# Optimization experiments

Measured on AMD Instinct MI355X. Metric: run time of the kernel, lower is better.

The kernel has to match this reference:

```python
import jax, jax.numpy as jnp
import numpy as np
from jax import lax

WIN = 9  # box-filter window per spatial dim
PAD = WIN // 2


def _box_sum(x, filt):
    # x: [N,1,D,H,W]; uniform ones filter -> local sums, 'same' padding
    return lax.conv_general_dilated(
        x, filt, window_strides=(1, 1, 1),
        padding=[(PAD, PAD)] * 3,
        dimension_numbers=("NCDHW", "OIDHW", "NCDHW"))


def l_ncc(I, J):
    filt = jnp.ones((1, 1, WIN, WIN, WIN), dtype=I.dtype)
    win_size = float(WIN ** 3)
    I_sum = _box_sum(I, filt)
    J_sum = _box_sum(J, filt)
    I2_sum = _box_sum(I * I, filt)
    J2_sum = _box_sum(J * J, filt)
    IJ_sum = _box_sum(I * J, filt)
    u_I = I_sum / win_size
    u_J = J_sum / win_size
    cross = IJ_sum - u_J * I_sum - u_I * J_sum + u_I * u_J * win_size
    I_var = I2_sum - 2.0 * u_I * I_sum + u_I * u_I * win_size
    J_var = J2_sum - 2.0 * u_J * J_sum + u_J * u_J * win_size
    cc = cross * cross / (I_var * J_var + 1e-5)
    return 1.0 - jnp.mean(cc)


def l_mse(y_true, y_pred):
    return jnp.mean((y_true - y_pred) ** 2)


def l_smooth(s):
    # squared forward differences along the three spatial axes of [N,C,D,H,W]
    dy = s[..., 1:, :, :] - s[..., :-1, :, :]
    dx = s[..., :, 1:, :] - s[..., :, :-1, :]
    dz = s[..., :, :, 1:] - s[..., :, :, :-1]
    d = jnp.mean(dx * dx) + jnp.mean(dy * dy) + jnp.mean(dz * dz)
    return d / 3.0


def setup_inputs() -> dict:
    key = jax.random.key(0)
    k1, k2, k3, k4 = jax.random.split(key, 4)
    shp = (2, 1, 128, 128, 128)
    return {
        "imgsA": jax.random.uniform(k1, shp, dtype=jnp.float32),
        "recon_A": jax.random.uniform(k2, shp, dtype=jnp.float32),
        "warped_BA": jax.random.uniform(k3, shp, dtype=jnp.float32),
        "flow_BA": jax.random.normal(k4, (2, 3, 128, 128, 128), dtype=jnp.float32),
    }


def reference(imgsA, recon_A, warped_BA, flow_BA):
    ncc_loss = l_ncc(warped_BA, imgsA)
    mse_loss = l_mse(imgsA, recon_A)
    smooth_loss = l_smooth(flow_BA)
    return (ncc_loss, mse_loss, smooth_loss)
```

## Files before the change

### kernel.cpp

```cpp
#include <hip/hip_runtime.h>

#define VOL   4194304
#define FLOWN 12582912
#define SMCNT 12484608.0f
#define WIN_INV (1.0f / 729.0f)

__device__ __forceinline__ void block_reduce_atomic(float v, float* red, float* dst) {
#pragma unroll
    for (int off = 32; off; off >>= 1) v += __shfl_down(v, off);
    if ((threadIdx.x & 63) == 0) red[threadIdx.x >> 6] = v;
    __syncthreads();
    if (threadIdx.x == 0) atomicAdd(dst, red[0] + red[1] + red[2] + red[3]);
}

struct __align__(16) NccLds {
    float wst[2][5][16][28];
    float hst[2][5][16][16];
};

#define WSLIDE(c, X0,X1,X2,X3,X4,X5,X6,X7,X8,X9,X10,X11)                   \
    {                                                                      \
        const float o0 = X0+X1+X2+X3+X4+X5+X6+X7+X8;                       \
        const float o1 = o0 - X0 + X9;                                     \
        const float o2 = o1 - X1 + X10;                                    \
        const float o3 = o2 - X2 + X11;                                    \
        L->wst[wpl][c][wq4 + 0][wrr] = o0;                                 \
        L->wst[wpl][c][wq4 + 1][wrr] = o1;                                 \
        L->wst[wpl][c][wq4 + 2][wrr] = o2;                                 \
        L->wst[wpl][c][wq4 + 3][wrr] = o3;                                 \
    }

__device__ void ncc_block(const float* __restrict__ I, const float* __restrict__ J,
                          float* __restrict__ acc, NccLds* L, float* red, int nb) {
    const int wt = nb & 7, ht = (nb >> 3) & 7, dc = (nb >> 6) & 7, n = nb >> 9;
    const int w0 = wt << 4, h0 = ht << 4, d0 = dc << 4;
    const int tid = threadIdx.x;
    const int th = tid & 15;
    const int tw = tid >> 4;

    const int wpl = tid / 96;
    const int wit = tid - wpl * 96;
    const int wrr = wit >> 2;
    const int wq4 = (wit & 3) << 2;
    const int gh  = h0 - 4 + wrr;
    const int gwb = w0 + wq4 - 4;

    float hist[5][9];
#pragma unroll
    for (int c = 0; c < 5; ++c)
#pragma unroll
        for (int k = 0; k < 9; ++k) hist[c][k] = 0.f;
    float S[5] = {0.f, 0.f, 0.f, 0.f, 0.f};
    float local = 0.f;
    const long nbase = (long)n * 2097152;

    for (int pp = 0; pp < 12; ++pp) {
        {
            const int s  = 2 * pp + wpl;
            const int dp = d0 - 4 + s;
            if (tid < 192 && (unsigned)dp < 128u) {
                const float4 z4 = make_float4(0.f, 0.f, 0.f, 0.f);
                float4 i0 = z4, i1 = z4, i2 = z4, j0 = z4, j1 = z4, j2 = z4;
                if ((unsigned)gh < 128u) {
                    const float* Ip = I + nbase + (long)dp * 16384 + gh * 128 + gwb;
                    const float* Jp = J + nbase + (long)dp * 16384 + gh * 128 + gwb;
                    if (gwb >= 0)   { i0 = *(const float4*)Ip;       j0 = *(const float4*)Jp; }
                    i1 = *(const float4*)(Ip + 4);                   j1 = *(const float4*)(Jp + 4);
                    if (gwb <= 116) { i2 = *(const float4*)(Ip + 8); j2 = *(const float4*)(Jp + 8); }
                }
                WSLIDE(0, i0.x,i0.y,i0.z,i0.w, i1.x,i1.y,i1.z,i1.w, i2.x,i2.y,i2.z,i2.w)
                WSLIDE(1, j0.x,j0.y,j0.z,j0.w, j1.x,j1.y,j1.z,j1.w, j2.x,j2.y,j2.z,j2.w)
                WSLIDE(2, i0.x*i0.x,i0.y*i0.y,i0.z*i0.z,i0.w*i0.w,
                          i1.x*i1.x,i1.y*i1.y,i1.z*i1.z,i1.w*i1.w,
                          i2.x*i2.x,i2.y*i2.y,i2.z*i2.z,i2.w*i2.w)
                WSLIDE(3, j0.x*j0.x,j0.y*j0.y,j0.z*j0.z,j0.w*j0.w,
                          j1.x*j1.x,j1.y*j1.y,j1.z*j1.z,j1.w*j1.w,
                          j2.x*j2.x,j2.y*j2.y,j2.z*j2.z,j2.w*j2.w)
                WSLIDE(4, i0.x*j0.x,i0.y*j0.y,i0.z*j0.z,i0.w*j0.w,
                          i1.x*j1.x,i1.y*j1.y,i1.z*j1.z,i1.w*j1.w,
                          i2.x*j2.x,i2.y*j2.y,i2.z*j2.z,i2.w*j2.w)
            }
        }
        __syncthreads();
#pragma unroll
        for (int rep = 0; rep < 3; ++rep) {
            int id = -1;
            if (rep < 2) id = tid + rep * 256;
            else if (tid >= 128) id = 384 + tid;
            if (id >= 0 && id < 640) {
                const int pl = id >= 320;
                const int r2 = id - pl * 320;
                const int c  = r2 >> 6;
                const int w  = (r2 >> 2) & 15;
                const int qh = r2 & 3;
                const int dp = d0 - 4 + 2 * pp + pl;
                if ((unsigned)dp < 128u) {
                    const float* sp = &L->wst[pl][c][w][qh << 2];
                    const float4 a0 = *(const float4*)sp;
                    const float4 a1 = *(const float4*)(sp + 4);
                    const float4 a2 = *(const float4*)(sp + 8);
                    const float o0 = a0.x+a0.y+a0.z+a0.w+a1.x+a1.y+a1.z+a1.w+a2.x;
                    const float o1 = o0 - a0.x + a2.y;
                    const float o2 = o1 - a0.y + a2.z;
                    const float o3 = o2 - a0.z + a2.w;
                    *(float4*)&L->hst[pl][c][w][qh << 2] = make_float4(o0, o1, o2, o3);
                }
            }
        }
        __syncthreads();
        {
            const int dp0 = d0 - 4 + 2 * pp;
            float p0[5], p1[5];
            if ((unsigned)dp0 < 128u) {
#pragma unroll
                for (int c = 0; c < 5; ++c) p0[c] = L->hst[0][c][tw][th];
            } else {
#pragma unroll
                for (int c = 0; c < 5; ++c) p0[c] = 0.f;
            }
            if ((unsigned)(dp0 + 1) < 128u) {
#pragma unroll
                for (int c = 0; c < 5; ++c) p1[c] = L->hst[1][c][tw][th];
            } else {
#pragma unroll
                for (int c = 0; c < 5; ++c) p1[c] = 0.f;
            }
#pragma unroll
            for (int c = 0; c < 5; ++c) S[c] += p0[c] - hist[c][8];
            if (pp >= 4) {
                const float cross = S[4] - S[0] * S[1] * WIN_INV;
                const float iv    = S[2] - S[0] * S[0] * WIN_INV;
                const float jv    = S[3] - S[1] * S[1] * WIN_INV;
                local += cross * cross / (iv * jv + 1e-5f);
            }
#pragma unroll
            for (int c = 0; c < 5; ++c) S[c] += p1[c] - hist[c][7];
            if (pp >= 4) {
                const float cross = S[4] - S[0] * S[1] * WIN_INV;
                const float iv    = S[2] - S[0] * S[0] * WIN_INV;
                const float jv    = S[3] - S[1] * S[1] * WIN_INV;
                local += cross * cross / (iv * jv + 1e-5f);
            }
#pragma unroll
            for (int c = 0; c < 5; ++c) {
#pragma unroll
                for (int k = 8; k >= 2; --k) hist[c][k] = hist[c][k - 2];
                hist[c][1] = p0[c];
                hist[c][0] = p1[c];
            }
        }
    }
    block_reduce_atomic(local, red, &acc[0]);
}

__device__ void mse_block(const float4* __restrict__ a, const float4* __restrict__ b,
                          float* __restrict__ acc, float* red, int mb) {
    float local = 0.f;
    for (int i = mb * 256 + threadIdx.x; i < VOL / 4; i += 512 * 256) {
        const float4 x = a[i], y = b[i];
        const float d0 = x.x - y.x, d1 = x.y - y.y, d2 = x.z - y.z, d3 = x.w - y.w;
        local += d0 * d0 + d1 * d1 + d2 * d2 + d3 * d3;
    }
    block_reduce_atomic(local, red, &acc[1]);
}

__device__ void smooth_block(const float4* __restrict__ s,
                             float* __restrict__ acc, float* red, int sb) {
    float local = 0.f;
    for (int f = sb * 256 + threadIdx.x; f < FLOWN / 4; f += 2048 * 256) {
        const int w4 = f & 31, h = (f >> 5) & 127, d = (f >> 12) & 127;
        const float4 v = s[f];
        const float t1 = v.y - v.x, t2 = v.z - v.y, t3 = v.w - v.z;
        local += t1 * t1 + t2 * t2 + t3 * t3;
        if (w4 < 31) {
            const float nx = ((const float*)s)[4 * f + 4];
            const float t = nx - v.w;
            local += t * t;
        }
        if (h < 127) {
            const float4 nh = s[f + 32];
            const float u0 = nh.x - v.x, u1 = nh.y - v.y, u2 = nh.z - v.z, u3 = nh.w - v.w;
            local += u0 * u0 + u1 * u1 + u2 * u2 + u3 * u3;
        }
        if (d < 127) {
            const float4 nd = s[f + 4096];
            const float u0 = nd.x - v.x, u1 = nd.y - v.y, u2 = nd.z - v.z, u3 = nd.w - v.w;
            local += u0 * u0 + u1 * u1 + u2 * u2 + u3 * u3;
        }
    }
    block_reduce_atomic(local, red, &acc[2]);
}

__global__ __launch_bounds__(256) void fused_k(const float* __restrict__ imgsA,
                                               const float* __restrict__ recon,
                                               const float* __restrict__ warped,
                                               const float* __restrict__ flow,
                                               float* __restrict__ acc) {
    __shared__ NccLds Lsh;
    __shared__ float red[4];
    const int g = blockIdx.x;
    if (g < 1024) {
        ncc_block(warped, imgsA, acc, &Lsh, red, g);
    } else {
        const int x = g - 1024;
        const int q = x / 5, r = x - q * 5;
        if (r == 0) mse_block((const float4*)imgsA, (const float4*)recon, acc, red, q);
        else        smooth_block((const float4*)flow, acc, red, q * 4 + (r - 1));
    }
}

__global__ void fin_k(const float* __restrict__ acc, float* __restrict__ out) {
    if (threadIdx.x == 0) {
        out[0] = 1.0f - acc[0] * (1.0f / (float)VOL);
        out[1] = acc[1] * (1.0f / (float)VOL);
        out[2] = acc[2] * (1.0f / (3.0f * SMCNT));
    }
}

extern "C" void kernel_launch(void* const* d_in, const int* in_sizes, int n_in,
                              void* d_out, int out_size, void* d_ws, size_t ws_size,
                              hipStream_t stream) {
    const float* imgsA  = (const float*)d_in[0];
    const float* recon  = (const float*)d_in[1];
    const float* warped = (const float*)d_in[2];
    const float* flow   = (const float*)d_in[3];
    float* out = (float*)d_out;
    float* acc = (float*)d_ws;

    hipMemsetAsync(d_ws, 0, 16, stream);
    fused_k<<<3584, 256, 0, stream>>>(imgsA, recon, warped, flow, acc);
    fin_k<<<1, 64, 0, stream>>>(acc, out);
}
```

Measured before the change: 82.00 us.

## Process four depth planes per iteration with wave-local H pass and prefetch

The NCC box filter now gives each of the four waves its own depth plane, so four planes are handled per iteration instead of two. Each wave does the W-slide and the H-slide on its own plane using only a wave-local LDS wait, which removes one block-wide barrier per step. Global loads for the next plane group are issued into registers before the barrier, so memory traffic overlaps with the depth accumulation. Blocks are also interleaved so NCC blocks alternate with MSE and smooth blocks, and launch bounds request three blocks per CU. The cost is higher register use from the prefetch buffers and a larger LDS footprint, which could limit occupancy.

```diff
diff --git a/kernel.cpp b/kernel.cpp
--- a/kernel.cpp
+++ b/kernel.cpp
@@ -14,8 +14,8 @@
 }
 
 struct __align__(16) NccLds {
-    float wst[2][5][16][28];
-    float hst[2][5][16][16];
+    float wst[4][5][16][24];
+    float hst[4][5][16][16];
 };
 
 #define WSLIDE(c, X0,X1,X2,X3,X4,X5,X6,X7,X8,X9,X10,X11)                   \
@@ -24,10 +24,17 @@
         const float o1 = o0 - X0 + X9;                                     \
         const float o2 = o1 - X1 + X10;                                    \
         const float o3 = o2 - X2 + X11;                                    \
-        L->wst[wpl][c][wq4 + 0][wrr] = o0;                                 \
-        L->wst[wpl][c][wq4 + 1][wrr] = o1;                                 \
-        L->wst[wpl][c][wq4 + 2][wrr] = o2;                                 \
-        L->wst[wpl][c][wq4 + 3][wrr] = o3;                                 \
+        L->wst[wv][c][wq4 + 0][wrr] = o0;                                  \
+        L->wst[wv][c][wq4 + 1][wrr] = o1;                                  \
+        L->wst[wv][c][wq4 + 2][wrr] = o2;                                  \
+        L->wst[wv][c][wq4 + 3][wrr] = o3;                                  \
+    }
+
+#define EMIT {                                                             \
+        const float cross = S[4] - S[0] * S[1] * WIN_INV;                  \
+        const float iv    = S[2] - S[0] * S[0] * WIN_INV;                  \
+        const float jv    = S[3] - S[1] * S[1] * WIN_INV;                  \
+        local += cross * cross / (iv * jv + 1e-5f);                       \
     }
 
 __device__ void ncc_block(const float* __restrict__ I, const float* __restrict__ J,
@@ -35,15 +42,10 @@
     const int wt = nb & 7, ht = (nb >> 3) & 7, dc = (nb >> 6) & 7, n = nb >> 9;
     const int w0 = wt << 4, h0 = ht << 4, d0 = dc << 4;
     const int tid = threadIdx.x;
-    const int th = tid & 15;
-    const int tw = tid >> 4;
-
-    const int wpl = tid / 96;
-    const int wit = tid - wpl * 96;
-    const int wrr = wit >> 2;
-    const int wq4 = (wit & 3) << 2;
-    const int gh  = h0 - 4 + wrr;
-    const int gwb = w0 + wq4 - 4;
+    const int wv   = tid >> 6;
+    const int lane = tid & 63;
+    const int th = tid & 15, tw = (tid >> 4) & 15;
+    const int hw = (lane >> 2) & 15, hq = lane & 3;
 
     float hist[5][9];
 #pragma unroll
@@ -54,101 +56,103 @@
     float local = 0.f;
     const long nbase = (long)n * 2097152;
 
-    for (int pp = 0; pp < 12; ++pp) {
-        {
-            const int s  = 2 * pp + wpl;
-            const int dp = d0 - 4 + s;
-            if (tid < 192 && (unsigned)dp < 128u) {
-                const float4 z4 = make_float4(0.f, 0.f, 0.f, 0.f);
-                float4 i0 = z4, i1 = z4, i2 = z4, j0 = z4, j1 = z4, j2 = z4;
+    float4 Ri0[2], Ri1[2], Ri2[2], Rj0[2], Rj1[2], Rj2[2];
+
+    auto load_plane = [&](int s4) {
+        const int dp = d0 - 4 + s4 + wv;
+        const bool v = (unsigned)dp < 128u;
+#pragma unroll
+        for (int r = 0; r < 2; ++r) {
+            const float4 z4 = make_float4(0.f, 0.f, 0.f, 0.f);
+            Ri0[r] = Ri1[r] = Ri2[r] = Rj0[r] = Rj1[r] = Rj2[r] = z4;
+            const int item = lane + (r << 6);
+            if (v && item < 96) {
+                const int rr = item >> 2, q4 = (item & 3) << 2;
+                const int gh = h0 - 4 + rr, gwb = w0 + q4 - 4;
                 if ((unsigned)gh < 128u) {
                     const float* Ip = I + nbase + (long)dp * 16384 + gh * 128 + gwb;
                     const float* Jp = J + nbase + (long)dp * 16384 + gh * 128 + gwb;
-                    if (gwb >= 0)   { i0 = *(const float4*)Ip;       j0 = *(const float4*)Jp; }
-                    i1 = *(const float4*)(Ip + 4);                   j1 = *(const float4*)(Jp + 4);
-                    if (gwb <= 116) { i2 = *(const float4*)(Ip + 8); j2 = *(const float4*)(Jp + 8); }
-                }
-                WSLIDE(0, i0.x,i0.y,i0.z,i0.w, i1.x,i1.y,i1.z,i1.w, i2.x,i2.y,i2.z,i2.w)
-                WSLIDE(1, j0.x,j0.y,j0.z,j0.w, j1.x,j1.y,j1.z,j1.w, j2.x,j2.y,j2.z,j2.w)
-                WSLIDE(2, i0.x*i0.x,i0.y*i0.y,i0.z*i0.z,i0.w*i0.w,
-                          i1.x*i1.x,i1.y*i1.y,i1.z*i1.z,i1.w*i1.w,
-                          i2.x*i2.x,i2.y*i2.y,i2.z*i2.z,i2.w*i2.w)
-                WSLIDE(3, j0.x*j0.x,j0.y*j0.y,j0.z*j0.z,j0.w*j0.w,
-                          j1.x*j1.x,j1.y*j1.y,j1.z*j1.z,j1.w*j1.w,
-                          j2.x*j2.x,j2.y*j2.y,j2.z*j2.z,j2.w*j2.w)
-                WSLIDE(4, i0.x*j0.x,i0.y*j0.y,i0.z*j0.z,i0.w*j0.w,
-                          i1.x*j1.x,i1.y*j1.y,i1.z*j1.z,i1.w*j1.w,
-                          i2.x*j2.x,i2.y*j2.y,i2.z*j2.z,i2.w*j2.w)
-            }
-        }
-        __syncthreads();
-#pragma unroll
-        for (int rep = 0; rep < 3; ++rep) {
-            int id = -1;
-            if (rep < 2) id = tid + rep * 256;
-            else if (tid >= 128) id = 384 + tid;
-            if (id >= 0 && id < 640) {
-                const int pl = id >= 320;
-                const int r2 = id - pl * 320;
-                const int c  = r2 >> 6;
-                const int w  = (r2 >> 2) & 15;
-                const int qh = r2 & 3;
-                const int dp = d0 - 4 + 2 * pp + pl;
-                if ((unsigned)dp < 128u) {
-                    const float* sp = &L->wst[pl][c][w][qh << 2];
-                    const float4 a0 = *(const float4*)sp;
-                    const float4 a1 = *(const float4*)(sp + 4);
-                    const float4 a2 = *(const float4*)(sp + 8);
-                    const float o0 = a0.x+a0.y+a0.z+a0.w+a1.x+a1.y+a1.z+a1.w+a2.x;
-                    const float o1 = o0 - a0.x + a2.y;
-                    const float o2 = o1 - a0.y + a2.z;
-                    const float o3 = o2 - a0.z + a2.w;
-                    *(float4*)&L->hst[pl][c][w][qh << 2] = make_float4(o0, o1, o2, o3);
+                    if (gwb >= 0)   { Ri0[r] = *(const float4*)Ip;       Rj0[r] = *(const float4*)Jp; }
+                    Ri1[r] = *(const float4*)(Ip + 4);                   Rj1[r] = *(const float4*)(Jp + 4);
+                    if (gwb <= 116) { Ri2[r] = *(const float4*)(Ip + 8); Rj2[r] = *(const float4*)(Jp + 8); }
                 }
             }
         }
+    };
+
+    load_plane(0);
+    for (int pp = 0; pp < 6; ++pp) {
+        const int dpw = d0 - 4 + 4 * pp + wv;
+        const bool vpl = (unsigned)dpw < 128u;
+        if (vpl) {
+#pragma unroll
+            for (int r = 0; r < 2; ++r) {
+                const int item = lane + (r << 6);
+                if (item < 96) {
+                    const int wrr = item >> 2, wq4 = (item & 3) << 2;
+                    const float4 i0 = Ri0[r], i1 = Ri1[r], i2 = Ri2[r];
+                    const float4 j0 = Rj0[r], j1 = Rj1[r], j2 = Rj2[r];
+                    WSLIDE(0, i0.x,i0.y,i0.z,i0.w, i1.x,i1.y,i1.z,i1.w, i2.x,i2.y,i2.z,i2.w)
+                    WSLIDE(1, j0.x,j0.y,j0.z,j0.w, j1.x,j1.y,j1.z,j1.w, j2.x,j2.y,j2.z,j2.w)
+                    WSLIDE(2, i0.x*i0.x,i0.y*i0.y,i0.z*i0.z,i0.w*i0.w,
+                              i1.x*i1.x,i1.y*i1.y,i1.z*i1.z,i1.w*i1.w,
+                              i2.x*i2.x,i2.y*i2.y,i2.z*i2.z,i2.w*i2.w)
+                    WSLIDE(3, j0.x*j0.x,j0.y*j0.y,j0.z*j0.z,j0.w*j0.w,
+                              j1.x*j1.x,j1.y*j1.y,j1.z*j1.z,j1.w*j1.w,
+                              j2.x*j2.x,j2.y*j2.y,j2.z*j2.z,j2.w*j2.w)
+                    WSLIDE(4, i0.x*j0.x,i0.y*j0.y,i0.z*j0.z,i0.w*j0.w,
+                              i1.x*j1.x,i1.y*j1.y,i1.z*j1.z,i1.w*j1.w,
+                              i2.x*j2.x,i2.y*j2.y,i2.z*j2.z,i2.w*j2.w)
+                }
+            }
+        }
+        asm volatile("s_waitcnt lgkmcnt(0)" ::: "memory");
+        __builtin_amdgcn_sched_barrier(0);
+        if (vpl) {
+#pragma unroll
+            for (int c = 0; c < 5; ++c) {
+                const float* sp = &L->wst[wv][c][hw][hq << 2];
+                const float4 a0 = *(const float4*)sp;
+                const float4 a1 = *(const float4*)(sp + 4);
+                const float4 a2 = *(const float4*)(sp + 8);
+                const float o0 = a0.x+a0.y+a0.z+a0.w+a1.x+a1.y+a1.z+a1.w+a2.x;
+                const float o1 = o0 - a0.x + a2.y;
+                const float o2 = o1 - a0.y + a2.z;
+                const float o3 = o2 - a0.z + a2.w;
+                *(float4*)&L->hst[wv][c][hw][hq << 2] = make_float4(o0, o1, o2, o3);
+            }
+        }
+        if (pp < 5) load_plane(4 * (pp + 1));
         __syncthreads();
-        {
-            const int dp0 = d0 - 4 + 2 * pp;
-            float p0[5], p1[5];
-            if ((unsigned)dp0 < 128u) {
-#pragma unroll
-                for (int c = 0; c < 5; ++c) p0[c] = L->hst[0][c][tw][th];
-            } else {
-#pragma unroll
-                for (int c = 0; c < 5; ++c) p0[c] = 0.f;
-            }
-            if ((unsigned)(dp0 + 1) < 128u) {
-#pragma unroll
-                for (int c = 0; c < 5; ++c) p1[c] = L->hst[1][c][tw][th];
-            } else {
-#pragma unroll
-                for (int c = 0; c < 5; ++c) p1[c] = 0.f;
-            }
-#pragma unroll
-            for (int c = 0; c < 5; ++c) S[c] += p0[c] - hist[c][8];
-            if (pp >= 4) {
-                const float cross = S[4] - S[0] * S[1] * WIN_INV;
-                const float iv    = S[2] - S[0] * S[0] * WIN_INV;
-                const float jv    = S[3] - S[1] * S[1] * WIN_INV;
-                local += cross * cross / (iv * jv + 1e-5f);
-            }
-#pragma unroll
-            for (int c = 0; c < 5; ++c) S[c] += p1[c] - hist[c][7];
-            if (pp >= 4) {
-                const float cross = S[4] - S[0] * S[1] * WIN_INV;
-                const float iv    = S[2] - S[0] * S[0] * WIN_INV;
-                const float jv    = S[3] - S[1] * S[1] * WIN_INV;
-                local += cross * cross / (iv * jv + 1e-5f);
-            }
-#pragma unroll
-            for (int c = 0; c < 5; ++c) {
-#pragma unroll
-                for (int k = 8; k >= 2; --k) hist[c][k] = hist[c][k - 2];
-                hist[c][1] = p0[c];
-                hist[c][0] = p1[c];
-            }
-        }
+        float p[4][5];
+#pragma unroll
+        for (int q = 0; q < 4; ++q) {
+            const bool v = (unsigned)(d0 - 4 + 4 * pp + q) < 128u;
+#pragma unroll
+            for (int c = 0; c < 5; ++c)
+                p[q][c] = v ? L->hst[q][c][tw][th] : 0.f;
+        }
+#pragma unroll
+        for (int c = 0; c < 5; ++c) S[c] += p[0][c] - hist[c][8];
+        if (pp >= 2) EMIT
+#pragma unroll
+        for (int c = 0; c < 5; ++c) S[c] += p[1][c] - hist[c][7];
+        if (pp >= 2) EMIT
+#pragma unroll
+        for (int c = 0; c < 5; ++c) S[c] += p[2][c] - hist[c][6];
+        if (pp >= 2) EMIT
+#pragma unroll
+        for (int c = 0; c < 5; ++c) S[c] += p[3][c] - hist[c][5];
+        if (pp >= 2) EMIT
+#pragma unroll
+        for (int c = 0; c < 5; ++c) {
+            hist[c][8] = hist[c][4]; hist[c][7] = hist[c][3];
+            hist[c][6] = hist[c][2]; hist[c][5] = hist[c][1];
+            hist[c][4] = hist[c][0];
+            hist[c][3] = p[0][c];    hist[c][2] = p[1][c];
+            hist[c][1] = p[2][c];    hist[c][0] = p[3][c];
+        }
+        __syncthreads();
     }
     block_reduce_atomic(local, red, &acc[0]);
 }
@@ -191,21 +195,21 @@
     block_reduce_atomic(local, red, &acc[2]);
 }
 
-__global__ __launch_bounds__(256) void fused_k(const float* __restrict__ imgsA,
-                                               const float* __restrict__ recon,
-                                               const float* __restrict__ warped,
-                                               const float* __restrict__ flow,
-                                               float* __restrict__ acc) {
+__global__ __launch_bounds__(256, 3) void fused_k(const float* __restrict__ imgsA,
+                                                  const float* __restrict__ recon,
+                                                  const float* __restrict__ warped,
+                                                  const float* __restrict__ flow,
+                                                  float* __restrict__ acc) {
     __shared__ NccLds Lsh;
     __shared__ float red[4];
     const int g = blockIdx.x;
-    if (g < 1024) {
-        ncc_block(warped, imgsA, acc, &Lsh, red, g);
+    const int r7 = g % 7, q7 = g / 7;
+    if (r7 < 2) {
+        ncc_block(warped, imgsA, acc, &Lsh, red, q7 * 2 + r7);
     } else {
-        const int x = g - 1024;
-        const int q = x / 5, r = x - q * 5;
-        if (r == 0) mse_block((const float4*)imgsA, (const float4*)recon, acc, red, q);
-        else        smooth_block((const float4*)flow, acc, red, q * 4 + (r - 1));
+        const int mb = q7 * 5 + (r7 - 2);
+        if (mb < 512) mse_block((const float4*)imgsA, (const float4*)recon, acc, red, mb);
+        else          smooth_block((const float4*)flow, acc, red, mb - 512);
     }
 }
 
```

Measured after the change: 82.12 us. Within noise of the previous version (+0.1%).

## Prefetch next NCC depth slab, pad LDS, interleave block roles, cap occupancy

Applied to the files above, without the earlier changes.

Global loads for the next pair of depth planes are now issued into registers before the barrier and the LDS-based box-sum reduction, so memory latency overlaps with the current plane's compute. The h-stage LDS array gets row padding to reduce bank conflicts. Block IDs now interleave NCC blocks with MSE and smoothness blocks in a 2:5 pattern instead of running all NCC blocks first, which mixes compute-heavy and bandwidth-heavy work across CUs. A launch-bounds minimum-blocks hint is added, which may constrain register allocation and cause spills given the extra prefetch registers.

```diff
diff --git a/kernel.cpp b/kernel.cpp
--- a/kernel.cpp
+++ b/kernel.cpp
@@ -15,7 +15,7 @@
 
 struct __align__(16) NccLds {
     float wst[2][5][16][28];
-    float hst[2][5][16][16];
+    float hst[2][5][16][20];
 };
 
 #define WSLIDE(c, X0,X1,X2,X3,X4,X5,X6,X7,X8,X9,X10,X11)                   \
@@ -30,6 +30,13 @@
         L->wst[wpl][c][wq4 + 3][wrr] = o3;                                 \
     }
 
+#define EMIT {                                                             \
+        const float cross = S[4] - S[0] * S[1] * WIN_INV;                  \
+        const float iv    = S[2] - S[0] * S[0] * WIN_INV;                  \
+        const float jv    = S[3] - S[1] * S[1] * WIN_INV;                  \
+        local += cross * cross / (iv * jv + 1e-5f);                       \
+    }
+
 __device__ void ncc_block(const float* __restrict__ I, const float* __restrict__ J,
                           float* __restrict__ acc, NccLds* L, float* red, int nb) {
     const int wt = nb & 7, ht = (nb >> 3) & 7, dc = (nb >> 6) & 7, n = nb >> 9;
@@ -44,6 +51,7 @@
     const int wq4 = (wit & 3) << 2;
     const int gh  = h0 - 4 + wrr;
     const int gwb = w0 + wq4 - 4;
+    const bool wthr = (tid < 192) && ((unsigned)gh < 128u);
 
     float hist[5][9];
 #pragma unroll
@@ -54,20 +62,28 @@
     float local = 0.f;
     const long nbase = (long)n * 2097152;
 
+    float4 Pi0, Pi1, Pi2, Pj0, Pj1, Pj2;
+
+    auto issue_loads = [&](int pp) {
+        const int dp = d0 - 4 + 2 * pp + wpl;
+        const float4 z4 = make_float4(0.f, 0.f, 0.f, 0.f);
+        Pi0 = Pi1 = Pi2 = Pj0 = Pj1 = Pj2 = z4;
+        if (wthr && (unsigned)dp < 128u) {
+            const float* Ip = I + nbase + (long)dp * 16384 + gh * 128 + gwb;
+            const float* Jp = J + nbase + (long)dp * 16384 + gh * 128 + gwb;
+            if (gwb >= 0)   { Pi0 = *(const float4*)Ip;       Pj0 = *(const float4*)Jp; }
+            Pi1 = *(const float4*)(Ip + 4);                   Pj1 = *(const float4*)(Jp + 4);
+            if (gwb <= 116) { Pi2 = *(const float4*)(Ip + 8); Pj2 = *(const float4*)(Jp + 8); }
+        }
+    };
+
+    issue_loads(0);
     for (int pp = 0; pp < 12; ++pp) {
         {
-            const int s  = 2 * pp + wpl;
-            const int dp = d0 - 4 + s;
+            const int dp = d0 - 4 + 2 * pp + wpl;
             if (tid < 192 && (unsigned)dp < 128u) {
-                const float4 z4 = make_float4(0.f, 0.f, 0.f, 0.f);
-                float4 i0 = z4, i1 = z4, i2 = z4, j0 = z4, j1 = z4, j2 = z4;
-                if ((unsigned)gh < 128u) {
-                    const float* Ip = I + nbase + (long)dp * 16384 + gh * 128 + gwb;
-                    const float* Jp = J + nbase + (long)dp * 16384 + gh * 128 + gwb;
-                    if (gwb >= 0)   { i0 = *(const float4*)Ip;       j0 = *(const float4*)Jp; }
-                    i1 = *(const float4*)(Ip + 4);                   j1 = *(const float4*)(Jp + 4);
-                    if (gwb <= 116) { i2 = *(const float4*)(Ip + 8); j2 = *(const float4*)(Jp + 8); }
-                }
+                const float4 i0 = Pi0, i1 = Pi1, i2 = Pi2;
+                const float4 j0 = Pj0, j1 = Pj1, j2 = Pj2;
                 WSLIDE(0, i0.x,i0.y,i0.z,i0.w, i1.x,i1.y,i1.z,i1.w, i2.x,i2.y,i2.z,i2.w)
                 WSLIDE(1, j0.x,j0.y,j0.z,j0.w, j1.x,j1.y,j1.z,j1.w, j2.x,j2.y,j2.z,j2.w)
                 WSLIDE(2, i0.x*i0.x,i0.y*i0.y,i0.z*i0.z,i0.w*i0.w,
@@ -81,6 +97,7 @@
                           i2.x*j2.x,i2.y*j2.y,i2.z*j2.z,i2.w*j2.w)
             }
         }
+        if (pp < 11) issue_loads(pp + 1);
         __syncthreads();
 #pragma unroll
         for (int rep = 0; rep < 3; ++rep) {
@@ -127,24 +144,16 @@
             }
 #pragma unroll
             for (int c = 0; c < 5; ++c) S[c] += p0[c] - hist[c][8];
-            if (pp >= 4) {
-                const float cross = S[4] - S[0] * S[1] * WIN_INV;
-                const float iv    = S[2] - S[0] * S[0] * WIN_INV;
-                const float jv    = S[3] - S[1] * S[1] * WIN_INV;
-                local += cross * cross / (iv * jv + 1e-5f);
-            }
+            if (pp >= 4) EMIT
 #pragma unroll
             for (int c = 0; c < 5; ++c) S[c] += p1[c] - hist[c][7];
-            if (pp >= 4) {
-                const float cross = S[4] - S[0] * S[1] * WIN_INV;
-                const float iv    = S[2] - S[0] * S[0] * WIN_INV;
-                const float jv    = S[3] - S[1] * S[1] * WIN_INV;
-                local += cross * cross / (iv * jv + 1e-5f);
-            }
+            if (pp >= 4) EMIT
 #pragma unroll
             for (int c = 0; c < 5; ++c) {
-#pragma unroll
-                for (int k = 8; k >= 2; --k) hist[c][k] = hist[c][k - 2];
+                hist[c][8] = hist[c][6]; hist[c][7] = hist[c][5];
+                hist[c][6] = hist[c][4]; hist[c][5] = hist[c][3];
+                hist[c][4] = hist[c][2]; hist[c][3] = hist[c][1];
+                hist[c][2] = hist[c][0];
                 hist[c][1] = p0[c];
                 hist[c][0] = p1[c];
             }
@@ -191,21 +200,21 @@
     block_reduce_atomic(local, red, &acc[2]);
 }
 
-__global__ __launch_bounds__(256) void fused_k(const float* __restrict__ imgsA,
-                                               const float* __restrict__ recon,
-                                               const float* __restrict__ warped,
-                                               const float* __restrict__ flow,
-                                               float* __restrict__ acc) {
+__global__ __launch_bounds__(256, 5) void fused_k(const float* __restrict__ imgsA,
+                                                  const float* __restrict__ recon,
+                                                  const float* __restrict__ warped,
+                                                  const float* __restrict__ flow,
+                                                  float* __restrict__ acc) {
     __shared__ NccLds Lsh;
     __shared__ float red[4];
     const int g = blockIdx.x;
-    if (g < 1024) {
-        ncc_block(warped, imgsA, acc, &Lsh, red, g);
+    const int r7 = g % 7, q7 = g / 7;
+    if (r7 < 2) {
+        ncc_block(warped, imgsA, acc, &Lsh, red, q7 * 2 + r7);
     } else {
-        const int x = g - 1024;
-        const int q = x / 5, r = x - q * 5;
-        if (r == 0) mse_block((const float4*)imgsA, (const float4*)recon, acc, red, q);
-        else        smooth_block((const float4*)flow, acc, red, q * 4 + (r - 1));
+        const int mb = q7 * 5 + (r7 - 2);
+        if (mb < 512) mse_block((const float4*)imgsA, (const float4*)recon, acc, red, mb);
+        else          smooth_block((const float4*)flow, acc, red, mb - 512);
     }
 }
 
```

New measurement: 89.55 us. 9.2% more time.

## Enlarge NCC depth tile, unroll with ring-buffer history, interleave block roles

Applied to the files above, without the earlier changes.

Each NCC block now covers 32 output depth planes instead of 16. That lowers the share of redundant halo planes each block loads and box-filters, and halves the number of NCC blocks. The depth loop is fully unrolled, and the 9-deep history shift is replaced by a modulo-indexed ring buffer whose indices become compile-time constants, removing register moves. The grid also interleaves NCC, MSE and smooth blocks so that heavy and light work mix across CUs. The costs are larger code and more register pressure from the full unroll, plus longer per-block tails because there are fewer, bigger NCC blocks.

```diff
diff --git a/kernel.cpp b/kernel.cpp
--- a/kernel.cpp
+++ b/kernel.cpp
@@ -30,10 +30,17 @@
         L->wst[wpl][c][wq4 + 3][wrr] = o3;                                 \
     }
 
+#define EMIT {                                                             \
+        const float cross = S[4] - S[0] * S[1] * WIN_INV;                  \
+        const float iv    = S[2] - S[0] * S[0] * WIN_INV;                  \
+        const float jv    = S[3] - S[1] * S[1] * WIN_INV;                  \
+        local += cross * cross / (iv * jv + 1e-5f);                       \
+    }
+
 __device__ void ncc_block(const float* __restrict__ I, const float* __restrict__ J,
                           float* __restrict__ acc, NccLds* L, float* red, int nb) {
-    const int wt = nb & 7, ht = (nb >> 3) & 7, dc = (nb >> 6) & 7, n = nb >> 9;
-    const int w0 = wt << 4, h0 = ht << 4, d0 = dc << 4;
+    const int wt = nb & 7, ht = (nb >> 3) & 7, dc = (nb >> 6) & 3, n = nb >> 8;
+    const int w0 = wt << 4, h0 = ht << 4, d0 = dc << 5;
     const int tid = threadIdx.x;
     const int th = tid & 15;
     const int tw = tid >> 4;
@@ -44,6 +51,7 @@
     const int wq4 = (wit & 3) << 2;
     const int gh  = h0 - 4 + wrr;
     const int gwb = w0 + wq4 - 4;
+    const bool wthr = (tid < 192) && ((unsigned)gh < 128u);
 
     float hist[5][9];
 #pragma unroll
@@ -54,20 +62,18 @@
     float local = 0.f;
     const long nbase = (long)n * 2097152;
 
-    for (int pp = 0; pp < 12; ++pp) {
+#pragma unroll
+    for (int pp = 0; pp < 20; ++pp) {
         {
-            const int s  = 2 * pp + wpl;
-            const int dp = d0 - 4 + s;
-            if (tid < 192 && (unsigned)dp < 128u) {
+            const int dp = d0 - 4 + 2 * pp + wpl;
+            if (wthr && (unsigned)dp < 128u) {
                 const float4 z4 = make_float4(0.f, 0.f, 0.f, 0.f);
                 float4 i0 = z4, i1 = z4, i2 = z4, j0 = z4, j1 = z4, j2 = z4;
-                if ((unsigned)gh < 128u) {
-                    const float* Ip = I + nbase + (long)dp * 16384 + gh * 128 + gwb;
-                    const float* Jp = J + nbase + (long)dp * 16384 + gh * 128 + gwb;
-                    if (gwb >= 0)   { i0 = *(const float4*)Ip;       j0 = *(const float4*)Jp; }
-                    i1 = *(const float4*)(Ip + 4);                   j1 = *(const float4*)(Jp + 4);
-                    if (gwb <= 116) { i2 = *(const float4*)(Ip + 8); j2 = *(const float4*)(Jp + 8); }
-                }
+                const float* Ip = I + nbase + (long)dp * 16384 + gh * 128 + gwb;
+                const float* Jp = J + nbase + (long)dp * 16384 + gh * 128 + gwb;
+                if (gwb >= 0)   { i0 = *(const float4*)Ip;       j0 = *(const float4*)Jp; }
+                i1 = *(const float4*)(Ip + 4);                   j1 = *(const float4*)(Jp + 4);
+                if (gwb <= 116) { i2 = *(const float4*)(Ip + 8); j2 = *(const float4*)(Jp + 8); }
                 WSLIDE(0, i0.x,i0.y,i0.z,i0.w, i1.x,i1.y,i1.z,i1.w, i2.x,i2.y,i2.z,i2.w)
                 WSLIDE(1, j0.x,j0.y,j0.z,j0.w, j1.x,j1.y,j1.z,j1.w, j2.x,j2.y,j2.z,j2.w)
                 WSLIDE(2, i0.x*i0.x,i0.y*i0.y,i0.z*i0.z,i0.w*i0.w,
@@ -109,7 +115,9 @@
         }
         __syncthreads();
         {
-            const int dp0 = d0 - 4 + 2 * pp;
+            const int s0 = 2 * pp, s1 = 2 * pp + 1;
+            const int k0 = s0 % 9, k1 = s1 % 9;
+            const int dp0 = d0 - 4 + s0;
             float p0[5], p1[5];
             if ((unsigned)dp0 < 128u) {
 #pragma unroll
@@ -126,28 +134,17 @@
                 for (int c = 0; c < 5; ++c) p1[c] = 0.f;
             }
 #pragma unroll
-            for (int c = 0; c < 5; ++c) S[c] += p0[c] - hist[c][8];
-            if (pp >= 4) {
-                const float cross = S[4] - S[0] * S[1] * WIN_INV;
-                const float iv    = S[2] - S[0] * S[0] * WIN_INV;
-                const float jv    = S[3] - S[1] * S[1] * WIN_INV;
-                local += cross * cross / (iv * jv + 1e-5f);
-            }
-#pragma unroll
-            for (int c = 0; c < 5; ++c) S[c] += p1[c] - hist[c][7];
-            if (pp >= 4) {
-                const float cross = S[4] - S[0] * S[1] * WIN_INV;
-                const float iv    = S[2] - S[0] * S[0] * WIN_INV;
-                const float jv    = S[3] - S[1] * S[1] * WIN_INV;
-                local += cross * cross / (iv * jv + 1e-5f);
-            }
-#pragma unroll
             for (int c = 0; c < 5; ++c) {
-#pragma unroll
-                for (int k = 8; k >= 2; --k) hist[c][k] = hist[c][k - 2];
-                hist[c][1] = p0[c];
-                hist[c][0] = p1[c];
-            }
+                S[c] += p0[c] - hist[c][k0];
+                hist[c][k0] = p0[c];
+            }
+            if (s0 >= 8) EMIT
+#pragma unroll
+            for (int c = 0; c < 5; ++c) {
+                S[c] += p1[c] - hist[c][k1];
+                hist[c][k1] = p1[c];
+            }
+            if (s1 >= 8) EMIT
         }
     }
     block_reduce_atomic(local, red, &acc[0]);
@@ -199,14 +196,10 @@
     __shared__ NccLds Lsh;
     __shared__ float red[4];
     const int g = blockIdx.x;
-    if (g < 1024) {
-        ncc_block(warped, imgsA, acc, &Lsh, red, g);
-    } else {
-        const int x = g - 1024;
-        const int q = x / 5, r = x - q * 5;
-        if (r == 0) mse_block((const float4*)imgsA, (const float4*)recon, acc, red, q);
-        else        smooth_block((const float4*)flow, acc, red, q * 4 + (r - 1));
-    }
+    const int r6 = g % 6, q6 = g / 6;
+    if (r6 == 0)      ncc_block(warped, imgsA, acc, &Lsh, red, q6);
+    else if (r6 == 1) mse_block((const float4*)imgsA, (const float4*)recon, acc, red, q6);
+    else              smooth_block((const float4*)flow, acc, red, q6 * 4 + (r6 - 2));
 }
 
 __global__ void fin_k(const float* __restrict__ acc, float* __restrict__ out) {
@@ -228,6 +221,6 @@
     float* acc = (float*)d_ws;
 
     hipMemsetAsync(d_ws, 0, 16, stream);
-    fused_k<<<3584, 256, 0, stream>>>(imgsA, recon, warped, flow, acc);
+    fused_k<<<3072, 256, 0, stream>>>(imgsA, recon, warped, flow, acc);
     fin_k<<<1, 64, 0, stream>>>(acc, out);
 }
```

Result: slower. 115.2 us (+40.5%).
